# Performance work log

Measured on AMD Instinct MI355X. Metric: run time of the kernel, lower is better.

## Reference

```python
import jax, jax.numpy as jnp
import numpy as np

EMB, NH, NG, T_MAX = 2048, 16, 4, 2048
HD = EMB // NH          # 128
HPG = NH // NG          # 4
B, T = 2, 2048


def _rope_tables(t):
    inv_freq = 1.0 / (10000.0 ** (jnp.arange(0, HD, 2, dtype=jnp.float32) / HD))
    freqs = jnp.outer(jnp.arange(t, dtype=jnp.float32), inv_freq)  # [t, HD//2]
    return jnp.cos(freqs), jnp.sin(freqs)


def _apply_rope(x, cos, sin):
    # x: [..., t, HD], interleaved pairs (0::2 real, 1::2 imag)
    x1 = x[..., 0::2]
    x2 = x[..., 1::2]
    r1 = x1 * cos - x2 * sin
    r2 = x1 * sin + x2 * cos
    return jnp.stack([r1, r2], axis=-1).reshape(x.shape)


def setup_inputs() -> dict:
    key = jax.random.key(0)
    ks = jax.random.split(key, 5)
    s = 0.02
    return {
        "x": jax.random.normal(ks[0], (B, T, EMB), dtype=jnp.float32),
        "Wq": jax.random.normal(ks[1], (EMB, EMB), dtype=jnp.float32) * s,
        "Wk": jax.random.normal(ks[2], (NG * HD, EMB), dtype=jnp.float32) * s,
        "Wv": jax.random.normal(ks[3], (NG * HD, EMB), dtype=jnp.float32) * s,
        "Wo": jax.random.normal(ks[4], (EMB, EMB), dtype=jnp.float32) * s,
    }


def reference(x, Wq, Wk, Wv, Wo):
    b, t, _ = x.shape
    cos, sin = _rope_tables(t)  # [t, HD//2] each; broadcast over batch/heads

    # projections (torch Linear: x @ W.T)
    q = (x @ Wq.T).reshape(b, t, NH, HD).transpose(0, 2, 1, 3)  # [b, NH, t, HD]
    k = (x @ Wk.T).reshape(b, t, NG, HD).transpose(0, 2, 1, 3)  # [b, NG, t, HD]
    v = (x @ Wv.T).reshape(b, t, NG, HD).transpose(0, 2, 1, 3)  # [b, NG, t, HD]

    q = _apply_rope(q, cos, sin)
    k = _apply_rope(k, cos, sin)

    # grouped attention without materializing expanded K/V
    qg = q.reshape(b, NG, HPG, t, HD)                       # [b, g, h, t, d]
    scale = 1.0 / jnp.sqrt(jnp.asarray(HD, dtype=x.dtype))
    scores = jnp.einsum('bghtd,bgsd->bghts', qg, k) * scale  # [b, g, h, t, s]

    causal = jnp.tril(jnp.ones((t, t), dtype=bool))
    scores = jnp.where(causal, scores, jnp.finfo(scores.dtype).min)
    attn = jax.nn.softmax(scores, axis=-1)

    out = jnp.einsum('bghts,bgsd->bghtd', attn, v)           # [b, g, h, t, d]
    out = out.reshape(b, NH, t, HD).transpose(0, 2, 1, 3).reshape(b, t, EMB)
    return out @ Wo.T
```

## Files before the change

### kernel.cpp

```cpp
#include <hip/hip_runtime.h>
#include <stdint.h>
#include <math.h>

#define EMB 2048
#define NHq 16
#define NGk 4
#define HD 128
#define Bb 2
#define Tt 2048
#define MROWS (Bb*Tt)
#define QKVN 3072
#define NQT 32

typedef __bf16 bf16x8 __attribute__((ext_vector_type(8)));
typedef float f32x4 __attribute__((ext_vector_type(4)));
typedef unsigned short u16;

__device__ __forceinline__ u16 f2bf(float f) {
    unsigned int u = __float_as_uint(f);
    u += 0x7fff + ((u >> 16) & 1);
    return (u16)(u >> 16);
}

__device__ __forceinline__ unsigned int cvt_pk_bf16(float lo, float hi) {
    unsigned int r;
    asm("v_cvt_pk_bf16_f32 %0, %1, %2" : "=v"(r) : "v"(lo), "v"(hi));
    return r;
}

#define GLOAD_LDS16(g, l) \
    __builtin_amdgcn_global_load_lds((const __attribute__((address_space(1))) void*)(g), \
                                     (__attribute__((address_space(3))) void*)(l), 16, 0, 0)

__global__ void cast_bf16_kernel(const float* __restrict__ src, u16* __restrict__ dst, int n4) {
    int i = blockIdx.x * blockDim.x + threadIdx.x;
    if (i < n4) {
        float4 v = reinterpret_cast<const float4*>(src)[i];
        ushort4 o;
        o.x = f2bf(v.x); o.y = f2bf(v.y); o.z = f2bf(v.z); o.w = f2bf(v.w);
        reinterpret_cast<ushort4*>(dst)[i] = o;
    }
}

__global__ void rope_tables_kernel(float* __restrict__ ctab, float* __restrict__ stab) {
    int t = blockIdx.x, i = threadIdx.x;
    float inv = powf(10000.f, -2.f * (float)i / (float)HD);
    float ang = (float)t * inv;
    ctab[t * 64 + i] = cosf(ang);
    stab[t * 64 + i] = sinf(ang);
}

__global__ void rope_kernel(const float* __restrict__ lin, const float* __restrict__ ctab,
                            const float* __restrict__ stab, u16* __restrict__ out,
                            int coloff, int nh, float scale) {
    int i = threadIdx.x;
    int tt = blockIdx.x * 4 + threadIdx.y;
    int h = blockIdx.y, b = blockIdx.z;
    const float2 xv = *reinterpret_cast<const float2*>(
        &lin[((size_t)(b * Tt + tt)) * QKVN + coloff + h * HD + 2 * i]);
    float c = ctab[tt * 64 + i], s = stab[tt * 64 + i];
    ushort2 o;
    o.x = f2bf((xv.x * c - xv.y * s) * scale);
    o.y = f2bf((xv.x * s + xv.y * c) * scale);
    *reinterpret_cast<ushort2*>(&out[(((size_t)(b * nh + h)) * Tt + tt) * HD + 2 * i]) = o;
}

__global__ void vtrans_kernel(const float* __restrict__ lin, u16* __restrict__ vt) {
    int tx = threadIdx.x, dy = threadIdx.y;
    int tt = blockIdx.x * 64 + tx;
    int g = blockIdx.y, b = blockIdx.z;
    int ttp = (tt & ~63) | (((tt & 15) << 2) | ((tt >> 4) & 3));
    const float* src = &lin[((size_t)(b * Tt + tt)) * QKVN + EMB + NGk * HD + g * HD];
    u16* dst = &vt[(((size_t)(b * NGk + g)) * HD) * Tt + ttp];
    #pragma unroll
    for (int k = 0; k < 16; ++k) {
        int d = dy + k * 8;
        dst[(size_t)d * Tt] = f2bf(src[d]);
    }
}

__global__ __launch_bounds__(256) void gemm_bt(const u16* __restrict__ A, const u16* __restrict__ W,
                                               float* __restrict__ C, int M, int N, int K) {
    __shared__ u16 Atile[128 * 32];
    __shared__ u16 Btile[128 * 32];
    const int brow = blockIdx.x * 128;
    const int bcol = blockIdx.y * 128;
    const int t = threadIdx.x;
    const int w = t >> 6, l = t & 63;
    const int lr = l & 15, lq = l >> 4;
    const int wr = (w >> 1) * 64, wc = (w & 1) * 64;
    f32x4 acc[4][4] = {};
    const int nkt = K >> 5;
    for (int kt = 0; kt < nkt; ++kt) {
        const int k0 = kt * 32;
        #pragma unroll
        for (int i = 0; i < 2; ++i) {
            int f = i * 256 + t;
            int row = f >> 2, cb = (f & 3) * 8;
            GLOAD_LDS16(A + (size_t)(brow + row) * K + k0 + cb, &Atile[(i * 256 + w * 64) * 8]);
            GLOAD_LDS16(W + (size_t)(bcol + row) * K + k0 + cb, &Btile[(i * 256 + w * 64) * 8]);
        }
        __syncthreads();
        bf16x8 a[4], b[4];
        #pragma unroll
        for (int m = 0; m < 4; ++m)
            a[m] = *reinterpret_cast<const bf16x8*>(&Atile[(wr + m * 16 + lr) * 32 + lq * 8]);
        #pragma unroll
        for (int n = 0; n < 4; ++n)
            b[n] = *reinterpret_cast<const bf16x8*>(&Btile[(wc + n * 16 + lr) * 32 + lq * 8]);
        #pragma unroll
        for (int m = 0; m < 4; ++m)
            #pragma unroll
            for (int n = 0; n < 4; ++n)
                acc[m][n] = __builtin_amdgcn_mfma_f32_16x16x32_bf16(a[m], b[n], acc[m][n], 0, 0, 0);
        __syncthreads();
    }
    #pragma unroll
    for (int m = 0; m < 4; ++m)
        #pragma unroll
        for (int n = 0; n < 4; ++n)
            #pragma unroll
            for (int r = 0; r < 4; ++r)
                C[(size_t)(brow + wr + m * 16 + lq * 4 + r) * N + bcol + wc + n * 16 + lr] = acc[m][n][r];
}

__global__ __launch_bounds__(256) void flash_attn(const u16* __restrict__ Q, const u16* __restrict__ K,
                                                  const u16* __restrict__ Vt, u16* __restrict__ Out) {
    __shared__ u16 Klds[2][64 * 128];
    __shared__ u16 Vlds[2][128 * 64];
    __shared__ u16 Plds[4][16 * 64];
    const int ilo = blockIdx.x;
    const int ihi = NQT - 1 - ilo;
    const int h = blockIdx.y;
    const int b = blockIdx.z;
    const int g = h >> 2;
    const int t = threadIdx.x;
    const int w = t >> 6, l = t & 63;
    const int lr = l & 15, lq = l >> 4;

    const size_t qhead = ((size_t)(b * NHq + h)) * Tt;
    const size_t qblo = (qhead + ilo * 64 + w * 16) * HD;
    const size_t qbhi = (qhead + ihi * 64 + w * 16) * HD;
    bf16x8 qfl[4], qfh[4];
    #pragma unroll
    for (int d = 0; d < 4; ++d) {
        qfl[d] = *reinterpret_cast<const bf16x8*>(&Q[qblo + (size_t)lr * HD + d * 32 + lq * 8]);
        qfh[d] = *reinterpret_cast<const bf16x8*>(&Q[qbhi + (size_t)lr * HD + d * 32 + lq * 8]);
    }
    bf16x8 ones;
    #pragma unroll
    for (int j = 0; j < 8; ++j) ones[j] = (__bf16)1.0f;

    f32x4 ol[8] = {}, oh[8] = {};
    f32x4 lsum_l = {}, lsum_h = {};

    const int qlo0 = ilo * 64 + w * 16 + lq * 4;
    const int qhi0 = ihi * 64 + w * 16 + lq * 4;
    const size_t kbase  = ((size_t)(b * NGk + g)) * Tt * HD;
    const size_t vtbase = ((size_t)(b * NGk + g)) * HD * Tt;
    const int nkt = NQT - ilo;

    int kofs[4], vofs[4];
    #pragma unroll
    for (int j = 0; j < 4; ++j) {
        int blk = j * 4 + w;
        int krow = blk * 4 + (l >> 4);
        int kcb = (l & 15) ^ (krow & 7);
        kofs[j] = krow * HD + kcb * 8;
        int vd = blk * 8 + (l >> 3);
        int vseg = (l & 7) ^ (vd & 7);
        vofs[j] = vd * Tt + vseg * 8;
    }

    #pragma unroll
    for (int j = 0; j < 4; ++j) {
        int blk = j * 4 + w;
        GLOAD_LDS16(K + kbase + kofs[j], &Klds[0][blk * 512]);
        GLOAD_LDS16(Vt + vtbase + vofs[j], &Vlds[0][blk * 512]);
    }
    int cur = 0;

    for (int kt = 0; kt < nkt; ++kt) {
        const int kp0 = kt * 64;
        __syncthreads();
        if (kt + 1 < nkt) {
            const int kp1 = kp0 + 64;
            #pragma unroll
            for (int j = 0; j < 4; ++j) {
                int blk = j * 4 + w;
                GLOAD_LDS16(K + kbase + (size_t)kp1 * HD + kofs[j], &Klds[cur ^ 1][blk * 512]);
                GLOAD_LDS16(Vt + vtbase + kp1 + vofs[j], &Vlds[cur ^ 1][blk * 512]);
            }
        }
        const u16* Kb = Klds[cur];
        const u16* Vb = Vlds[cur];

        const bool lo_act = (kt <= ilo);
        f32x4 sl[4] = {}, sh[4] = {};
        __builtin_amdgcn_s_setprio(1);
        #pragma unroll
        for (int ct = 0; ct < 4; ++ct) {
            #pragma unroll
            for (int d = 0; d < 4; ++d) {
                int row = ct * 16 + lr;
                int bo = row * 256 + ((d * 64 + lq * 16) ^ ((row & 7) << 4));
                bf16x8 kf = *reinterpret_cast<const bf16x8*>((const char*)Kb + bo);
                if (lo_act) sl[ct] = __builtin_amdgcn_mfma_f32_16x16x32_bf16(qfl[d], kf, sl[ct], 0, 0, 0);
                sh[ct] = __builtin_amdgcn_mfma_f32_16x16x32_bf16(qfh[d], kf, sh[ct], 0, 0, 0);
            }
        }
        __builtin_amdgcn_s_setprio(0);

        {
            const bool diag = (kt == nkt - 1);
            float e[4][4];
            #pragma unroll
            for (int ct = 0; ct < 4; ++ct)
                #pragma unroll
                for (int r = 0; r < 4; ++r) {
                    float v = sh[ct][r];
                    if (diag && (kp0 + ct * 16 + lr > qhi0 + r)) v = -1e30f;
                    e[ct][r] = exp2f(v);
                }
            #pragma unroll
            for (int r = 0; r < 4; ++r) {
                int row = lq * 4 + r;
                uint2 pk;
                pk.x = cvt_pk_bf16(e[0][r], e[1][r]);
                pk.y = cvt_pk_bf16(e[2][r], e[3][r]);
                int bo = row * 128 + ((lr * 8) ^ ((row & 7) << 4));
                *reinterpret_cast<uint2*>((char*)Plds[w] + bo) = pk;
            }
        }
        bf16x8 pfh0, pfh1;
        {
            int bo0 = lr * 128 + ((lq * 16) ^ ((lr & 7) << 4));
            int bo1 = lr * 128 + ((64 + lq * 16) ^ ((lr & 7) << 4));
            pfh0 = *reinterpret_cast<const bf16x8*>((const char*)Plds[w] + bo0);
            pfh1 = *reinterpret_cast<const bf16x8*>((const char*)Plds[w] + bo1);
        }
        bf16x8 pfl0, pfl1;
        if (lo_act) {
            const bool diag = (kt == ilo);
            float e[4][4];
            #pragma unroll
            for (int ct = 0; ct < 4; ++ct)
                #pragma unroll
                for (int r = 0; r < 4; ++r) {
                    float v = sl[ct][r];
                    if (diag && (kp0 + ct * 16 + lr > qlo0 + r)) v = -1e30f;
                    e[ct][r] = exp2f(v);
                }
            #pragma unroll
            for (int r = 0; r < 4; ++r) {
                int row = lq * 4 + r;
                uint2 pk;
                pk.x = cvt_pk_bf16(e[0][r], e[1][r]);
                pk.y = cvt_pk_bf16(e[2][r], e[3][r]);
                int bo = row * 128 + ((lr * 8) ^ ((row & 7) << 4));
                *reinterpret_cast<uint2*>((char*)Plds[w] + bo) = pk;
            }
            int bo0 = lr * 128 + ((lq * 16) ^ ((lr & 7) << 4));
            int bo1 = lr * 128 + ((64 + lq * 16) ^ ((lr & 7) << 4));
            pfl0 = *reinterpret_cast<const bf16x8*>((const char*)Plds[w] + bo0);
            pfl1 = *reinterpret_cast<const bf16x8*>((const char*)Plds[w] + bo1);
        }

        __builtin_amdgcn_s_setprio(1);
        #pragma unroll
        for (int n = 0; n < 8; ++n) {
            int dcol = n * 16 + lr;
            int bv0 = dcol * 128 + ((lq * 16) ^ ((dcol & 7) << 4));
            int bv1 = dcol * 128 + ((64 + lq * 16) ^ ((dcol & 7) << 4));
            bf16x8 vf0 = *reinterpret_cast<const bf16x8*>((const char*)Vb + bv0);
            bf16x8 vf1 = *reinterpret_cast<const bf16x8*>((const char*)Vb + bv1);
            oh[n] = __builtin_amdgcn_mfma_f32_16x16x32_bf16(pfh0, vf0, oh[n], 0, 0, 0);
            oh[n] = __builtin_amdgcn_mfma_f32_16x16x32_bf16(pfh1, vf1, oh[n], 0, 0, 0);
            if (lo_act) {
                ol[n] = __builtin_amdgcn_mfma_f32_16x16x32_bf16(pfl0, vf0, ol[n], 0, 0, 0);
                ol[n] = __builtin_amdgcn_mfma_f32_16x16x32_bf16(pfl1, vf1, ol[n], 0, 0, 0);
            }
        }
        lsum_h = __builtin_amdgcn_mfma_f32_16x16x32_bf16(pfh0, ones, lsum_h, 0, 0, 0);
        lsum_h = __builtin_amdgcn_mfma_f32_16x16x32_bf16(pfh1, ones, lsum_h, 0, 0, 0);
        if (lo_act) {
            lsum_l = __builtin_amdgcn_mfma_f32_16x16x32_bf16(pfl0, ones, lsum_l, 0, 0, 0);
            lsum_l = __builtin_amdgcn_mfma_f32_16x16x32_bf16(pfl1, ones, lsum_l, 0, 0, 0);
        }
        __builtin_amdgcn_s_setprio(0);
        cur ^= 1;
    }

    float invl[4], invh[4];
    #pragma unroll
    for (int r = 0; r < 4; ++r) { invl[r] = 1.f / lsum_l[r]; invh[r] = 1.f / lsum_h[r]; }
    const size_t obase = ((size_t)b * Tt) * EMB + (size_t)h * HD;
    #pragma unroll
    for (int n = 0; n < 8; ++n)
        #pragma unroll
        for (int r = 0; r < 4; ++r) {
            int rl = ilo * 64 + w * 16 + lq * 4 + r;
            int rh = ihi * 64 + w * 16 + lq * 4 + r;
            Out[obase + (size_t)rl * EMB + n * 16 + lr] = f2bf(ol[n][r] * invl[r]);
            Out[obase + (size_t)rh * EMB + n * 16 + lr] = f2bf(oh[n][r] * invh[r]);
        }
}

extern "C" void kernel_launch(void* const* d_in, const int* in_sizes, int n_in,
                              void* d_out, int out_size, void* d_ws, size_t ws_size,
                              hipStream_t stream) {
    (void)in_sizes; (void)n_in; (void)out_size; (void)ws_size;
    const float* x  = (const float*)d_in[0];
    const float* Wq = (const float*)d_in[1];
    const float* Wk = (const float*)d_in[2];
    const float* Wv = (const float*)d_in[3];
    const float* Wo = (const float*)d_in[4];
    float* out = (float*)d_out;

    char* ws = (char*)d_ws;
    size_t off = 0;
    auto alloc = [&](size_t bytes) { char* p = ws + off; off += (bytes + 255) & ~(size_t)255; return p; };

    u16* w_bf    = (u16*)alloc((size_t)(QKVN * EMB + EMB * EMB) * 2);
    u16* x_bf    = (u16*)alloc((size_t)MROWS * EMB * 2);
    float* qkv_lin = (float*)alloc((size_t)MROWS * QKVN * 4);
    u16* Qb      = (u16*)alloc((size_t)Bb * NHq * Tt * HD * 2);
    u16* Kb      = (u16*)alloc((size_t)Bb * NGk * Tt * HD * 2);
    u16* Vtb     = (u16*)alloc((size_t)Bb * NGk * HD * Tt * 2);
    float* ctab  = (float*)alloc((size_t)Tt * 64 * 4);
    float* stab  = (float*)alloc((size_t)Tt * 64 * 4);
    u16* attnout = (u16*)qkv_lin;

    u16* wq_bf = w_bf;
    u16* wk_bf = w_bf + (size_t)EMB * EMB;
    u16* wv_bf = wk_bf + (size_t)NGk * HD * EMB;
    u16* wo_bf = wv_bf + (size_t)NGk * HD * EMB;

    cast_bf16_kernel<<<(MROWS * EMB / 4 + 255) / 256, 256, 0, stream>>>(x, x_bf, MROWS * EMB / 4);
    cast_bf16_kernel<<<(EMB * EMB / 4 + 255) / 256, 256, 0, stream>>>(Wq, wq_bf, EMB * EMB / 4);
    cast_bf16_kernel<<<(NGk * HD * EMB / 4 + 255) / 256, 256, 0, stream>>>(Wk, wk_bf, NGk * HD * EMB / 4);
    cast_bf16_kernel<<<(NGk * HD * EMB / 4 + 255) / 256, 256, 0, stream>>>(Wv, wv_bf, NGk * HD * EMB / 4);
    cast_bf16_kernel<<<(EMB * EMB / 4 + 255) / 256, 256, 0, stream>>>(Wo, wo_bf, EMB * EMB / 4);
    rope_tables_kernel<<<Tt, 64, 0, stream>>>(ctab, stab);

    gemm_bt<<<dim3(MROWS / 128, QKVN / 128), 256, 0, stream>>>(x_bf, w_bf, qkv_lin, MROWS, QKVN, EMB);

    const float qscale = 1.44269504088896f / sqrtf((float)HD);
    rope_kernel<<<dim3(Tt / 4, NHq, Bb), dim3(64, 4), 0, stream>>>(qkv_lin, ctab, stab, Qb, 0, NHq, qscale);
    rope_kernel<<<dim3(Tt / 4, NGk, Bb), dim3(64, 4), 0, stream>>>(qkv_lin, ctab, stab, Kb, EMB, NGk, 1.0f);
    vtrans_kernel<<<dim3(Tt / 64, NGk, Bb), dim3(64, 8), 0, stream>>>(qkv_lin, Vtb);

    flash_attn<<<dim3(NQT / 2, NHq, Bb), 256, 0, stream>>>(Qb, Kb, Vtb, attnout);

    gemm_bt<<<dim3(MROWS / 128, EMB / 128), 256, 0, stream>>>(attnout, wo_bf, out, MROWS, EMB, EMB);
}
```

Baseline: 257.7 us.

## Split attention KV range across two blocks with partial-sum reduce kernel

Each paired query-tile block is now split into two blocks that process alternating 32-key tiles (even/odd) and write unnormalized fp32 partial outputs and row sums to workspace. A new reduce kernel adds the two partials, normalizes, and writes the bf16 attention output, reusing the x_bf and Qb buffers. Key tile size drops from 64 to 32, with V transposed layout and LDS P staging changed to match. This doubles the grid to raise occupancy and parallelism, but adds fp32 partial write/read traffic, an extra launch, and halves MFMA work per sync step.

```diff
diff --git a/kernel.cpp b/kernel.cpp
--- a/kernel.cpp
+++ b/kernel.cpp
@@ -15,6 +15,7 @@
 typedef __bf16 bf16x8 __attribute__((ext_vector_type(8)));
 typedef float f32x4 __attribute__((ext_vector_type(4)));
 typedef unsigned short u16;
+typedef unsigned int u32;
 
 __device__ __forceinline__ u16 f2bf(float f) {
     unsigned int u = __float_as_uint(f);
@@ -22,8 +23,8 @@
     return (u16)(u >> 16);
 }
 
-__device__ __forceinline__ unsigned int cvt_pk_bf16(float lo, float hi) {
-    unsigned int r;
+__device__ __forceinline__ u32 cvt_pk_bf16(float lo, float hi) {
+    u32 r;
     asm("v_cvt_pk_bf16_f32 %0, %1, %2" : "=v"(r) : "v"(lo), "v"(hi));
     return r;
 }
@@ -69,7 +70,7 @@
     int tx = threadIdx.x, dy = threadIdx.y;
     int tt = blockIdx.x * 64 + tx;
     int g = blockIdx.y, b = blockIdx.z;
-    int ttp = (tt & ~63) | (((tt & 15) << 2) | ((tt >> 4) & 3));
+    int ttp = (tt & ~31) | (((tt & 15) << 1) | ((tt >> 4) & 1));
     const float* src = &lin[((size_t)(b * Tt + tt)) * QKVN + EMB + NGk * HD + g * HD];
     u16* dst = &vt[(((size_t)(b * NGk + g)) * HD) * Tt + ttp];
     #pragma unroll
@@ -125,11 +126,13 @@
 }
 
 __global__ __launch_bounds__(256) void flash_attn(const u16* __restrict__ Q, const u16* __restrict__ K,
-                                                  const u16* __restrict__ Vt, u16* __restrict__ Out) {
-    __shared__ u16 Klds[2][64 * 128];
-    __shared__ u16 Vlds[2][128 * 64];
-    __shared__ u16 Plds[4][16 * 64];
-    const int ilo = blockIdx.x;
+                                                  const u16* __restrict__ Vt,
+                                                  float* __restrict__ Opart, float* __restrict__ Lpart) {
+    __shared__ u16 Klds[2][32 * 128];
+    __shared__ u16 Vlds[2][128 * 32];
+    __shared__ u16 Plds[4][16 * 32];
+    const int ilo = blockIdx.x >> 1;
+    const int par = blockIdx.x & 1;
     const int ihi = NQT - 1 - ilo;
     const int h = blockIdx.y;
     const int b = blockIdx.z;
@@ -158,48 +161,48 @@
     const int qhi0 = ihi * 64 + w * 16 + lq * 4;
     const size_t kbase  = ((size_t)(b * NGk + g)) * Tt * HD;
     const size_t vtbase = ((size_t)(b * NGk + g)) * HD * Tt;
-    const int nkt = NQT - ilo;
-
-    int kofs[4], vofs[4];
-    #pragma unroll
-    for (int j = 0; j < 4; ++j) {
-        int blk = j * 4 + w;
-        int krow = blk * 4 + (l >> 4);
-        int kcb = (l & 15) ^ (krow & 7);
-        kofs[j] = krow * HD + kcb * 8;
-        int vd = blk * 8 + (l >> 3);
-        int vseg = (l & 7) ^ (vd & 7);
-        vofs[j] = vd * Tt + vseg * 8;
-    }
-
-    #pragma unroll
-    for (int j = 0; j < 4; ++j) {
-        int blk = j * 4 + w;
-        GLOAD_LDS16(K + kbase + kofs[j], &Klds[0][blk * 512]);
-        GLOAD_LDS16(Vt + vtbase + vofs[j], &Vlds[0][blk * 512]);
+    const int nsteps = NQT - ilo;
+
+    int kofs[2], vofs[2];
+    #pragma unroll
+    for (int j = 0; j < 2; ++j) {
+        int c = j * 256 + w * 64 + l;
+        int krow = c >> 4;
+        kofs[j] = krow * HD + ((l & 15) ^ (krow & 7)) * 8;
+        int vd = c >> 2;
+        vofs[j] = vd * Tt + (l & 3) * 8;
+    }
+
+    {
+        const size_t kp = (size_t)par * 32;
+        #pragma unroll
+        for (int j = 0; j < 2; ++j) {
+            GLOAD_LDS16(K + kbase + kp * HD + kofs[j], &Klds[0][j * 2048 + w * 512]);
+            GLOAD_LDS16(Vt + vtbase + kp + vofs[j], &Vlds[0][j * 2048 + w * 512]);
+        }
     }
     int cur = 0;
 
-    for (int kt = 0; kt < nkt; ++kt) {
-        const int kp0 = kt * 64;
+    for (int i = 0; i < nsteps; ++i) {
+        const int kt = par + 2 * i;
+        const int kp0 = kt * 32;
         __syncthreads();
-        if (kt + 1 < nkt) {
-            const int kp1 = kp0 + 64;
-            #pragma unroll
-            for (int j = 0; j < 4; ++j) {
-                int blk = j * 4 + w;
-                GLOAD_LDS16(K + kbase + (size_t)kp1 * HD + kofs[j], &Klds[cur ^ 1][blk * 512]);
-                GLOAD_LDS16(Vt + vtbase + kp1 + vofs[j], &Vlds[cur ^ 1][blk * 512]);
+        if (i + 1 < nsteps) {
+            const size_t kp = (size_t)(kt + 2) * 32;
+            #pragma unroll
+            for (int j = 0; j < 2; ++j) {
+                GLOAD_LDS16(K + kbase + kp * HD + kofs[j], &Klds[cur ^ 1][j * 2048 + w * 512]);
+                GLOAD_LDS16(Vt + vtbase + kp + vofs[j], &Vlds[cur ^ 1][j * 2048 + w * 512]);
             }
         }
         const u16* Kb = Klds[cur];
         const u16* Vb = Vlds[cur];
 
-        const bool lo_act = (kt <= ilo);
-        f32x4 sl[4] = {}, sh[4] = {};
+        const bool lo_act = (kt <= 2 * ilo + 1);
+        f32x4 sl[2] = {}, sh[2] = {};
         __builtin_amdgcn_s_setprio(1);
         #pragma unroll
-        for (int ct = 0; ct < 4; ++ct) {
+        for (int ct = 0; ct < 2; ++ct) {
             #pragma unroll
             for (int d = 0; d < 4; ++d) {
                 int row = ct * 16 + lr;
@@ -212,10 +215,10 @@
         __builtin_amdgcn_s_setprio(0);
 
         {
-            const bool diag = (kt == nkt - 1);
-            float e[4][4];
-            #pragma unroll
-            for (int ct = 0; ct < 4; ++ct)
+            const bool diag = (kt >= 2 * ihi);
+            float e[2][4];
+            #pragma unroll
+            for (int ct = 0; ct < 2; ++ct)
                 #pragma unroll
                 for (int r = 0; r < 4; ++r) {
                     float v = sh[ct][r];
@@ -225,26 +228,16 @@
             #pragma unroll
             for (int r = 0; r < 4; ++r) {
                 int row = lq * 4 + r;
-                uint2 pk;
-                pk.x = cvt_pk_bf16(e[0][r], e[1][r]);
-                pk.y = cvt_pk_bf16(e[2][r], e[3][r]);
-                int bo = row * 128 + ((lr * 8) ^ ((row & 7) << 4));
-                *reinterpret_cast<uint2*>((char*)Plds[w] + bo) = pk;
+                *reinterpret_cast<u32*>((char*)Plds[w] + row * 64 + lr * 4) = cvt_pk_bf16(e[0][r], e[1][r]);
             }
         }
-        bf16x8 pfh0, pfh1;
-        {
-            int bo0 = lr * 128 + ((lq * 16) ^ ((lr & 7) << 4));
-            int bo1 = lr * 128 + ((64 + lq * 16) ^ ((lr & 7) << 4));
-            pfh0 = *reinterpret_cast<const bf16x8*>((const char*)Plds[w] + bo0);
-            pfh1 = *reinterpret_cast<const bf16x8*>((const char*)Plds[w] + bo1);
-        }
-        bf16x8 pfl0, pfl1;
+        bf16x8 pfh = *reinterpret_cast<const bf16x8*>((const char*)Plds[w] + lr * 64 + lq * 16);
+        bf16x8 pfl;
         if (lo_act) {
-            const bool diag = (kt == ilo);
-            float e[4][4];
-            #pragma unroll
-            for (int ct = 0; ct < 4; ++ct)
+            const bool diag = (kt >= 2 * ilo);
+            float e[2][4];
+            #pragma unroll
+            for (int ct = 0; ct < 2; ++ct)
                 #pragma unroll
                 for (int r = 0; r < 4; ++r) {
                     float v = sl[ct][r];
@@ -254,56 +247,77 @@
             #pragma unroll
             for (int r = 0; r < 4; ++r) {
                 int row = lq * 4 + r;
-                uint2 pk;
-                pk.x = cvt_pk_bf16(e[0][r], e[1][r]);
-                pk.y = cvt_pk_bf16(e[2][r], e[3][r]);
-                int bo = row * 128 + ((lr * 8) ^ ((row & 7) << 4));
-                *reinterpret_cast<uint2*>((char*)Plds[w] + bo) = pk;
+                *reinterpret_cast<u32*>((char*)Plds[w] + row * 64 + lr * 4) = cvt_pk_bf16(e[0][r], e[1][r]);
             }
-            int bo0 = lr * 128 + ((lq * 16) ^ ((lr & 7) << 4));
-            int bo1 = lr * 128 + ((64 + lq * 16) ^ ((lr & 7) << 4));
-            pfl0 = *reinterpret_cast<const bf16x8*>((const char*)Plds[w] + bo0);
-            pfl1 = *reinterpret_cast<const bf16x8*>((const char*)Plds[w] + bo1);
+            pfl = *reinterpret_cast<const bf16x8*>((const char*)Plds[w] + lr * 64 + lq * 16);
         }
 
         __builtin_amdgcn_s_setprio(1);
         #pragma unroll
         for (int n = 0; n < 8; ++n) {
-            int dcol = n * 16 + lr;
-            int bv0 = dcol * 128 + ((lq * 16) ^ ((dcol & 7) << 4));
-            int bv1 = dcol * 128 + ((64 + lq * 16) ^ ((dcol & 7) << 4));
-            bf16x8 vf0 = *reinterpret_cast<const bf16x8*>((const char*)Vb + bv0);
-            bf16x8 vf1 = *reinterpret_cast<const bf16x8*>((const char*)Vb + bv1);
-            oh[n] = __builtin_amdgcn_mfma_f32_16x16x32_bf16(pfh0, vf0, oh[n], 0, 0, 0);
-            oh[n] = __builtin_amdgcn_mfma_f32_16x16x32_bf16(pfh1, vf1, oh[n], 0, 0, 0);
-            if (lo_act) {
-                ol[n] = __builtin_amdgcn_mfma_f32_16x16x32_bf16(pfl0, vf0, ol[n], 0, 0, 0);
-                ol[n] = __builtin_amdgcn_mfma_f32_16x16x32_bf16(pfl1, vf1, ol[n], 0, 0, 0);
-            }
-        }
-        lsum_h = __builtin_amdgcn_mfma_f32_16x16x32_bf16(pfh0, ones, lsum_h, 0, 0, 0);
-        lsum_h = __builtin_amdgcn_mfma_f32_16x16x32_bf16(pfh1, ones, lsum_h, 0, 0, 0);
-        if (lo_act) {
-            lsum_l = __builtin_amdgcn_mfma_f32_16x16x32_bf16(pfl0, ones, lsum_l, 0, 0, 0);
-            lsum_l = __builtin_amdgcn_mfma_f32_16x16x32_bf16(pfl1, ones, lsum_l, 0, 0, 0);
-        }
+            int bv = (n * 16 + lr) * 64 + lq * 16;
+            bf16x8 vf = *reinterpret_cast<const bf16x8*>((const char*)Vb + bv);
+            oh[n] = __builtin_amdgcn_mfma_f32_16x16x32_bf16(pfh, vf, oh[n], 0, 0, 0);
+            if (lo_act) ol[n] = __builtin_amdgcn_mfma_f32_16x16x32_bf16(pfl, vf, ol[n], 0, 0, 0);
+        }
+        lsum_h = __builtin_amdgcn_mfma_f32_16x16x32_bf16(pfh, ones, lsum_h, 0, 0, 0);
+        if (lo_act) lsum_l = __builtin_amdgcn_mfma_f32_16x16x32_bf16(pfl, ones, lsum_l, 0, 0, 0);
         __builtin_amdgcn_s_setprio(0);
         cur ^= 1;
     }
 
-    float invl[4], invh[4];
-    #pragma unroll
-    for (int r = 0; r < 4; ++r) { invl[r] = 1.f / lsum_l[r]; invh[r] = 1.f / lsum_h[r]; }
-    const size_t obase = ((size_t)b * Tt) * EMB + (size_t)h * HD;
+    const int pblk = (((b * NHq + h) * 16) + ilo) * 2 + par;
+    float* Po = Opart + (size_t)pblk * 16384;
     #pragma unroll
     for (int n = 0; n < 8; ++n)
         #pragma unroll
         for (int r = 0; r < 4; ++r) {
-            int rl = ilo * 64 + w * 16 + lq * 4 + r;
-            int rh = ihi * 64 + w * 16 + lq * 4 + r;
-            Out[obase + (size_t)rl * EMB + n * 16 + lr] = f2bf(ol[n][r] * invl[r]);
-            Out[obase + (size_t)rh * EMB + n * 16 + lr] = f2bf(oh[n][r] * invh[r]);
-        }
+            int row = w * 16 + lq * 4 + r, col = n * 16 + lr;
+            Po[row * 128 + col] = oh[n][r];
+            Po[(64 + row) * 128 + col] = ol[n][r];
+        }
+    if (lr == 0) {
+        float* Lp = Lpart + (size_t)pblk * 128;
+        #pragma unroll
+        for (int r = 0; r < 4; ++r) {
+            int row = w * 16 + lq * 4 + r;
+            Lp[row] = lsum_h[r];
+            Lp[64 + row] = lsum_l[r];
+        }
+    }
+}
+
+__global__ __launch_bounds__(256) void reduce_attn(const float* __restrict__ Opart,
+                                                   const float* __restrict__ Lpart,
+                                                   u16* __restrict__ Out) {
+    const int qb = blockIdx.x;
+    const int h = blockIdx.y, b = blockIdx.z;
+    const bool ishi = (qb >= 16);
+    const int ilo = ishi ? (NQT - 1 - qb) : qb;
+    const int rowoff = ishi ? 0 : 64;
+    const size_t pb = (((size_t)(b * NHq + h) * 16) + ilo) * 2;
+    const float* O0 = Opart + pb * 16384;
+    const float* O1 = O0 + 16384;
+    const float* L0 = Lpart + pb * 128;
+    const float* L1 = L0 + 128;
+    const int tid = threadIdx.x;
+    const int r = tid >> 2;
+    const int qtr = tid & 3;
+    const float inv = 1.f / (L0[rowoff + r] + L1[rowoff + r]);
+    const float* s0 = O0 + (rowoff + r) * 128 + qtr * 32;
+    const float* s1 = O1 + (rowoff + r) * 128 + qtr * 32;
+    u16* dst = Out + ((size_t)(b * Tt) + qb * 64 + r) * EMB + h * HD + qtr * 32;
+    #pragma unroll
+    for (int v = 0; v < 8; ++v) {
+        float4 a = reinterpret_cast<const float4*>(s0)[v];
+        float4 c = reinterpret_cast<const float4*>(s1)[v];
+        ushort4 o;
+        o.x = f2bf((a.x + c.x) * inv);
+        o.y = f2bf((a.y + c.y) * inv);
+        o.z = f2bf((a.z + c.z) * inv);
+        o.w = f2bf((a.w + c.w) * inv);
+        reinterpret_cast<ushort4*>(dst)[v] = o;
+    }
 }
 
 extern "C" void kernel_launch(void* const* d_in, const int* in_sizes, int n_in,
@@ -329,7 +343,10 @@
     u16* Vtb     = (u16*)alloc((size_t)Bb * NGk * HD * Tt * 2);
     float* ctab  = (float*)alloc((size_t)Tt * 64 * 4);
     float* stab  = (float*)alloc((size_t)Tt * 64 * 4);
-    u16* attnout = (u16*)qkv_lin;
+    float* lpart = (float*)alloc((size_t)1024 * 128 * 4);
+
+    float* opart = (float*)x_bf;
+    u16* attnout = Qb;
 
     u16* wq_bf = w_bf;
     u16* wk_bf = w_bf + (size_t)EMB * EMB;
@@ -350,7 +367,9 @@
     rope_kernel<<<dim3(Tt / 4, NGk, Bb), dim3(64, 4), 0, stream>>>(qkv_lin, ctab, stab, Kb, EMB, NGk, 1.0f);
     vtrans_kernel<<<dim3(Tt / 64, NGk, Bb), dim3(64, 8), 0, stream>>>(qkv_lin, Vtb);
 
-    flash_attn<<<dim3(NQT / 2, NHq, Bb), 256, 0, stream>>>(Qb, Kb, Vtb, attnout);
+    flash_attn<<<dim3(NQT, NHq, Bb), 256, 0, stream>>>(Qb, Kb, Vtb, opart, lpart);
+
+    reduce_attn<<<dim3(NQT, NHq, Bb), 256, 0, stream>>>(opart, lpart, attnout);
 
     gemm_bt<<<dim3(MROWS / 128, EMB / 128), 256, 0, stream>>>(attnout, wo_bf, out, MROWS, EMB, EMB);
 }
```

Result: slower. 302.0 us (+17.2%).
